# Performance work log

Hardware: AMD Instinct MI355X
Metric: run time of the kernel (lower is better)

## Reference

```python
import jax, jax.numpy as jnp
import numpy as np

N_USERS = 100000
N_ITEMS = 40000
N_NODES = N_USERS + N_ITEMS
D = 64
IMG_DIM = 2048
TXT_DIM = 384
N_EDGES = 1000000
N_LAYERS = 2
ALPHA = 0.2


def setup_inputs() -> dict:
    key = jax.random.key(0)
    ks = jax.random.split(key, 10)
    edge_index = jax.random.randint(ks[0], (2, N_EDGES), 0, N_NODES, dtype=jnp.int64 if jax.config.jax_enable_x64 else jnp.int32)
    edge_weight = jax.random.uniform(ks[1], (N_EDGES, 1), dtype=jnp.float32)
    image_feats = jax.random.normal(ks[2], (N_ITEMS, IMG_DIM), dtype=jnp.float32)
    text_feats = jax.random.normal(ks[3], (N_ITEMS, TXT_DIM), dtype=jnp.float32)
    s_img = 1.0 / np.sqrt(IMG_DIM)
    s_txt = 1.0 / np.sqrt(TXT_DIM)
    image_trs_w = jax.random.uniform(ks[4], (IMG_DIM, D), jnp.float32, -s_img, s_img)
    image_trs_b = jnp.zeros((D,), jnp.float32)
    text_trs_w = jax.random.uniform(ks[5], (TXT_DIM, D), jnp.float32, -s_txt, s_txt)
    text_trs_b = jnp.zeros((D,), jnp.float32)
    image_pref = jax.random.normal(ks[6], (N_USERS, D), jnp.float32) * 0.1
    text_pref = jax.random.normal(ks[7], (N_USERS, D), jnp.float32) * 0.1
    return {
        "edge_index": edge_index,
        "edge_weight": edge_weight,
        "image_feats": image_feats,
        "text_feats": text_feats,
        "image_trs_w": image_trs_w,
        "image_trs_b": image_trs_b,
        "text_trs_w": text_trs_w,
        "text_trs_b": text_trs_b,
        "image_pref": image_pref,
        "text_pref": text_pref,
    }


def _l2_normalize(x):
    # matches F.normalize(x, p=2, dim=1, eps=1e-12)
    n = jnp.linalg.norm(x, axis=1, keepdims=True)
    return x / jnp.maximum(n, 1e-12)


def _propagate(x, src, dst, w):
    # PyG 'add' aggregation: message = x[src] * w, scatter-add into dst
    msgs = x[src] * w  # [E, D]
    return jax.ops.segment_sum(msgs, dst, num_segments=N_NODES)


def reference(edge_index, edge_weight, image_feats, text_feats,
              image_trs_w, image_trs_b, text_trs_w, text_trs_b,
              image_pref, text_pref):
    src, dst = edge_index[0], edge_index[1]

    image_emb = _l2_normalize(image_feats @ image_trs_w + image_trs_b)
    text_emb = _l2_normalize(text_feats @ text_trs_w + text_trs_b)

    ego_img = jnp.concatenate([image_pref, image_emb], axis=0)  # [N, D]
    ego_txt = jnp.concatenate([text_pref, text_emb], axis=0)    # [N, D]

    for _ in range(N_LAYERS):
        ego_img = _propagate(ego_img, src, dst, edge_weight) + ALPHA * ego_img
        ego_txt = _propagate(ego_txt, src, dst, edge_weight) + ALPHA * ego_txt

    # stack final modality embeddings; rows 0:N_USERS are user preferences,
    # N_USERS: are item embeddings (torch.split boundary)
    return jnp.stack([ego_img, ego_txt], axis=0)  # [2, N, D]
```

## Files before the change

kernel.cpp:

```cpp
#include <hip/hip_runtime.h>

#define N_USERS 100000
#define N_ITEMS 40000
#define NN      140000
#define N_EDGES 1000000
#define ALPHA   0.2f

typedef short bf16x8 __attribute__((ext_vector_type(8)));
typedef float f32x4  __attribute__((ext_vector_type(4)));

__device__ __forceinline__ unsigned short f2b(float x) {
    unsigned u = __builtin_bit_cast(unsigned, x);
    unsigned r = (u + 0x7FFFu + ((u >> 16) & 1u)) >> 16;
    return (unsigned short)r;
}
__device__ __forceinline__ unsigned cvtpk(float lo, float hi) {
    unsigned r;
    asm("v_cvt_pk_bf16_f32 %0, %1, %2" : "=v"(r) : "v"(lo), "v"(hi));
    return r;
}
__device__ __forceinline__ float blo(unsigned u) { return __builtin_bit_cast(float, u << 16); }
__device__ __forceinline__ float bhi(unsigned u) { return __builtin_bit_cast(float, u & 0xFFFF0000u); }

__device__ __forceinline__ void gl_lds16(const void* g, void* l) {
    __builtin_amdgcn_global_load_lds(
        (const __attribute__((address_space(1))) void*)g,
        (__attribute__((address_space(3))) void*)l, 16, 0, 0);
}

#define PREP_CP   6250
#define PREP_CI   (PREP_CP + 512)
#define PREP_CT   (PREP_CI + 96)
#define PREP_ALL  (PREP_CT + 3907)

__device__ __forceinline__ int wt_pos(int k, int n) {
    return ((k >> 5) * 4 + (n >> 4)) * 512 + ((((k >> 3) & 3) * 16) + (n & 15)) * 8 + (k & 7);
}

__global__ __launch_bounds__(256)
void prep(const float* __restrict__ imgp, const float* __restrict__ txtp,
          unsigned short* __restrict__ X,
          const float* __restrict__ Wi, short* __restrict__ WtImg,
          const float* __restrict__ Wx, short* __restrict__ WtTxt,
          const int* __restrict__ ei, int* __restrict__ deg,
          int* __restrict__ rank)
{
    int b = blockIdx.x, t = threadIdx.x;
    if (b < PREP_CP) {
        int tid = b * 256 + t;
        if (tid >= N_USERS * 16) return;
        int i  = tid >> 4;
        int c8 = tid & 15;
        const float* src = (c8 < 8) ? &imgp[(size_t)i * 64 + c8 * 8]
                                    : &txtp[(size_t)i * 64 + (c8 - 8) * 8];
        float4 a = *reinterpret_cast<const float4*>(src);
        float4 c = *reinterpret_cast<const float4*>(src + 4);
        int4 o = make_int4((int)cvtpk(a.x, a.y), (int)cvtpk(a.z, a.w),
                           (int)cvtpk(c.x, c.y), (int)cvtpk(c.z, c.w));
        *reinterpret_cast<int4*>(&X[(size_t)i * 128 + c8 * 8]) = o;
    } else if (b < PREP_CI) {
        int tid = (b - PREP_CP) * 256 + t;
        int k = tid >> 6, n = tid & 63;
        WtImg[wt_pos(k, n)] = (short)f2b(Wi[tid]);
    } else if (b < PREP_CT) {
        int tid = (b - PREP_CI) * 256 + t;
        if (tid >= 384 * 64) return;
        int k = tid >> 6, n = tid & 63;
        WtTxt[wt_pos(k, n)] = (short)f2b(Wx[tid]);
    } else {
        int e = (b - PREP_CT) * 256 + t;
        if (e < N_EDGES) {
            int d = ei[N_EDGES + e];
            int r = atomicAdd(&deg[d], 1);
            rank[e] = r;
        }
    }
}

template<int K, int COLOFF>
__device__ __forceinline__
void gemm_body(int bx, const float* __restrict__ A, const short* __restrict__ Wt,
               const float* __restrict__ bias, unsigned short* __restrict__ X,
               float* ldsA, short* ldsB)
{
    constexpr int NT = K / 64;
    const int t    = threadIdx.x;
    const int wid  = t >> 6;
    const int lane = t & 63;
    const int lo   = lane & 15;
    const int g    = lane >> 4;
    const int r0   = bx * 64;

    f32x4 acc[4];
    #pragma unroll
    for (int ct = 0; ct < 4; ++ct) acc[ct] = (f32x4){0.f, 0.f, 0.f, 0.f};

    auto stage = [&](int buf, int kt) {
        int k0 = kt * 64;
        #pragma unroll
        for (int i = 0; i < 4; ++i) {
            int c     = i * 4 + wid;
            int row_t = c * 4 + g;
            int u_log = lo ^ (row_t & 15);
            const float* gp = A + (size_t)(r0 + row_t) * K + k0 + u_log * 4;
            gl_lds16(gp, ldsA + buf * 4096 + c * 256);
        }
        #pragma unroll
        for (int i2 = 0; i2 < 2; ++i2) {
            int c2 = i2 * 4 + wid;
            const short* gp = Wt + ((size_t)kt * 8 + c2) * 512 + lane * 8;
            gl_lds16(gp, ldsB + buf * 4096 + c2 * 512);
        }
    };

    auto compute = [&](int buf) {
        int row_t = wid * 16 + lo;
        const float* baseA = ldsA + buf * 4096 + row_t * 64;
        const short* baseB = ldsB + buf * 4096;
        #pragma unroll
        for (int m = 0; m < 2; ++m) {
            int u0 = (m * 8 + 2 * g) ^ lo;
            int u1 = (m * 8 + 2 * g + 1) ^ lo;
            float4 xa = *reinterpret_cast<const float4*>(baseA + u0 * 4);
            float4 ya = *reinterpret_cast<const float4*>(baseA + u1 * 4);
            int4 ai = make_int4((int)cvtpk(xa.x, xa.y), (int)cvtpk(xa.z, xa.w),
                                (int)cvtpk(ya.x, ya.y), (int)cvtpk(ya.z, ya.w));
            bf16x8 a = __builtin_bit_cast(bf16x8, ai);
            #pragma unroll
            for (int ct = 0; ct < 4; ++ct) {
                int4 w = *reinterpret_cast<const int4*>(baseB + (m * 4 + ct) * 512 + lane * 8);
                bf16x8 bb = __builtin_bit_cast(bf16x8, w);
                acc[ct] = __builtin_amdgcn_mfma_f32_16x16x32_bf16(a, bb, acc[ct], 0, 0, 0);
            }
        }
    };

    stage(0, 0);
    for (int kt = 0; kt < NT; ++kt) {
        if (kt + 1 < NT) {
            stage((kt + 1) & 1, kt + 1);
            asm volatile("s_waitcnt vmcnt(6)" ::: "memory");
        } else {
            asm volatile("s_waitcnt vmcnt(0)" ::: "memory");
        }
        __builtin_amdgcn_s_barrier();
        __builtin_amdgcn_sched_barrier(0);
        compute(kt & 1);
        __builtin_amdgcn_s_barrier();
    }

    float bia[4];
    #pragma unroll
    for (int ct = 0; ct < 4; ++ct) bia[ct] = bias[ct * 16 + lo];

    int r0w = r0 + wid * 16;
    #pragma unroll
    for (int r = 0; r < 4; ++r) {
        float v[4];
        float ss = 0.f;
        #pragma unroll
        for (int ct = 0; ct < 4; ++ct) { v[ct] = acc[ct][r] + bia[ct]; ss += v[ct] * v[ct]; }
        ss += __shfl_xor(ss, 1);
        ss += __shfl_xor(ss, 2);
        ss += __shfl_xor(ss, 4);
        ss += __shfl_xor(ss, 8);
        float sc = 1.0f / fmaxf(sqrtf(ss), 1e-12f);
        int grow = r0w + g * 4 + r;
        unsigned short* dst = &X[(size_t)(N_USERS + grow) * 128 + COLOFF + lo];
        #pragma unroll
        for (int ct = 0; ct < 4; ++ct) dst[ct * 16] = f2b(v[ct] * sc);
    }
}

__global__ __launch_bounds__(256)
void gemm_fill(const float* __restrict__ Ai, const short* __restrict__ WtImg,
               const float* __restrict__ bi,
               const float* __restrict__ Ax, const short* __restrict__ WtTxt,
               const float* __restrict__ bx, unsigned short* __restrict__ X,
               const int* __restrict__ ei, const float* __restrict__ ew,
               const int* __restrict__ row_ptr, const int* __restrict__ rank,
               int2* __restrict__ epk)
{
    __shared__ float ldsA[8192];
    __shared__ __align__(16) short ldsB[8192];
    int b = blockIdx.x;
    if (b < 625)       gemm_body<2048, 0 >(b, Ai, WtImg, bi, X, ldsA, ldsB);
    else if (b < 1250) gemm_body< 384, 64>(b - 625, Ax, WtTxt, bx, X, ldsA, ldsB);
    else {
        int e = (b - 1250) * 256 + threadIdx.x;
        if (e >= N_EDGES) return;
        int s = ei[e];
        int d = ei[N_EDGES + e];
        int p = row_ptr[d] + rank[e];
        epk[p] = make_int2(s, __builtin_bit_cast(int, ew[e]));
    }
}

__global__ void scan1(const int* __restrict__ deg, int* __restrict__ row_ptr,
                      int* __restrict__ blockSums)
{
    __shared__ int ts[256];
    int t = threadIdx.x, b = blockIdx.x;
    int base = b * 1024 + t * 4;
    int v[4]; int s = 0;
    #pragma unroll
    for (int j = 0; j < 4; j++) {
        v[j] = (base + j < NN) ? deg[base + j] : 0;
        s += v[j];
    }
    ts[t] = s;
    __syncthreads();
    for (int off = 1; off < 256; off <<= 1) {
        int x = (t >= off) ? ts[t - off] : 0;
        __syncthreads();
        ts[t] += x;
        __syncthreads();
    }
    int excl = ts[t] - s;
    int run = excl;
    #pragma unroll
    for (int j = 0; j < 4; j++) {
        if (base + j < NN) row_ptr[base + j] = run;
        run += v[j];
    }
    if (t == 255) blockSums[b] = ts[255];
}

__global__ void scan23(const int* __restrict__ blockSums, int* __restrict__ row_ptr)
{
    __shared__ int ts[256];
    int t = threadIdx.x, b = blockIdx.x;
    ts[t] = (t < b) ? blockSums[t] : 0;
    __syncthreads();
    for (int off = 128; off > 0; off >>= 1) {
        if (t < off) ts[t] += ts[t + off];
        __syncthreads();
    }
    int off0 = ts[0];
    int base = b * 1024 + t * 4;
    #pragma unroll
    for (int j = 0; j < 4; j++) {
        int idx = base + j;
        if (idx < NN) row_ptr[idx] += off0;
    }
    if (b == 0 && t == 0) row_ptr[NN] = N_EDGES;
}

template<bool FINAL>
__global__ __launch_bounds__(256)
void propagate(const unsigned short* __restrict__ Xin, const int* __restrict__ row_ptr,
               const int2* __restrict__ epk, void* __restrict__ outv)
{
    int wid  = threadIdx.x >> 6;
    int lane = threadIdx.x & 63;
    int node = blockIdx.x * 4 + wid;
    if (node >= NN) return;
    int e0 = row_ptr[node];
    int e1 = row_ptr[node + 1];
    float accx = 0.f, accy = 0.f;
    for (int base = e0; base < e1; base += 64) {
        int cnt = e1 - base; if (cnt > 64) cnt = 64;
        int sv = 0, wvb = 0;
        if (base + lane < e1) {
            int2 ev = epk[base + lane];
            sv = ev.x; wvb = ev.y;
        }
        float wv = __builtin_bit_cast(float, wvb);
        int i = 0;
        for (; i + 3 < cnt; i += 4) {
            int   s0 = __shfl(sv, i),     s1 = __shfl(sv, i + 1);
            int   s2 = __shfl(sv, i + 2), s3 = __shfl(sv, i + 3);
            float w0 = __shfl(wv, i),     w1 = __shfl(wv, i + 1);
            float w2 = __shfl(wv, i + 2), w3 = __shfl(wv, i + 3);
            unsigned u0 = *reinterpret_cast<const unsigned*>(&Xin[(size_t)s0 * 128 + lane * 2]);
            unsigned u1 = *reinterpret_cast<const unsigned*>(&Xin[(size_t)s1 * 128 + lane * 2]);
            unsigned u2 = *reinterpret_cast<const unsigned*>(&Xin[(size_t)s2 * 128 + lane * 2]);
            unsigned u3 = *reinterpret_cast<const unsigned*>(&Xin[(size_t)s3 * 128 + lane * 2]);
            accx = fmaf(w0, blo(u0), accx); accy = fmaf(w0, bhi(u0), accy);
            accx = fmaf(w1, blo(u1), accx); accy = fmaf(w1, bhi(u1), accy);
            accx = fmaf(w2, blo(u2), accx); accy = fmaf(w2, bhi(u2), accy);
            accx = fmaf(w3, blo(u3), accx); accy = fmaf(w3, bhi(u3), accy);
        }
        for (; i < cnt; ++i) {
            int   s0 = __shfl(sv, i);
            float w0 = __shfl(wv, i);
            unsigned u0 = *reinterpret_cast<const unsigned*>(&Xin[(size_t)s0 * 128 + lane * 2]);
            accx = fmaf(w0, blo(u0), accx); accy = fmaf(w0, bhi(u0), accy);
        }
    }
    unsigned us = *reinterpret_cast<const unsigned*>(&Xin[(size_t)node * 128 + lane * 2]);
    accx += ALPHA * blo(us);
    accy += ALPHA * bhi(us);
    if (!FINAL) {
        unsigned short* out = (unsigned short*)outv;
        *reinterpret_cast<unsigned*>(&out[(size_t)node * 128 + lane * 2]) = cvtpk(accx, accy);
    } else {
        float* out = (float*)outv;
        int d = lane * 2;
        float* dst = (d < 64) ? &out[(size_t)node * 64 + d]
                              : &out[(size_t)NN * 64 + (size_t)node * 64 + (d - 64)];
        *reinterpret_cast<float2*>(dst) = make_float2(accx, accy);
    }
}

extern "C" void kernel_launch(void* const* d_in, const int* in_sizes, int n_in,
                              void* d_out, int out_size, void* d_ws, size_t ws_size,
                              hipStream_t stream)
{
    const int*   ei       = (const int*)d_in[0];
    const float* ew       = (const float*)d_in[1];
    const float* img_feat = (const float*)d_in[2];
    const float* txt_feat = (const float*)d_in[3];
    const float* img_w    = (const float*)d_in[4];
    const float* img_b    = (const float*)d_in[5];
    const float* txt_w    = (const float*)d_in[6];
    const float* txt_b    = (const float*)d_in[7];
    const float* img_pref = (const float*)d_in[8];
    const float* txt_pref = (const float*)d_in[9];
    float* out = (float*)d_out;

    const size_t XBYTES = (size_t)NN * 128 * 2;
    char* ws = (char*)d_ws;
    size_t off = 0;
    auto alloc = [&](size_t bytes) -> void* {
        void* p = ws + off;
        off = (off + bytes + 255) & ~(size_t)255;
        return p;
    };
    unsigned short* Xa = (unsigned short*)alloc(XBYTES);
    unsigned short* Xb = (unsigned short*)alloc(XBYTES);
    int*   deg     = (int*)alloc((size_t)NN * 4);
    int*   row_ptr = (int*)alloc((size_t)(NN + 1) * 4);
    int*   rank    = (int*)alloc((size_t)N_EDGES * 4);
    int2*  epk     = (int2*)alloc((size_t)N_EDGES * 8);
    int*   bsums   = (int*)alloc(256 * 4);
    short* WtImg   = (short*)alloc((size_t)2048 * 64 * 2);
    short* WtTxt   = (short*)alloc((size_t)384 * 64 * 2);

    hipMemsetAsync(deg, 0, (size_t)NN * 4, stream);

    prep<<<PREP_ALL, 256, 0, stream>>>(img_pref, txt_pref, Xa,
                                       img_w, WtImg, txt_w, WtTxt, ei, deg, rank);

    scan1<<<137, 256, 0, stream>>>(deg, row_ptr, bsums);
    scan23<<<137, 256, 0, stream>>>(bsums, row_ptr);

    gemm_fill<<<1250 + 3907, 256, 0, stream>>>(img_feat, WtImg, img_b,
                                               txt_feat, WtTxt, txt_b, Xa,
                                               ei, ew, row_ptr, rank, epk);

    propagate<false><<<35000, 256, 0, stream>>>(Xa, row_ptr, epk, Xb);
    propagate<true ><<<35000, 256, 0, stream>>>(Xb, row_ptr, epk, out);
}
```

Before: 305.4 us.

## Assign 16 lanes per node with 16-byte gathers in propagation

```diff
diff --git a/kernel.cpp b/kernel.cpp
--- a/kernel.cpp
+++ b/kernel.cpp
@@ -251,55 +251,70 @@
 void propagate(const unsigned short* __restrict__ Xin, const int* __restrict__ row_ptr,
                const int2* __restrict__ epk, void* __restrict__ outv)
 {
-    int wid  = threadIdx.x >> 6;
     int lane = threadIdx.x & 63;
-    int node = blockIdx.x * 4 + wid;
-    if (node >= NN) return;
+    int gl   = lane & 15;
+    int gb   = lane & 48;
+    int node = blockIdx.x * 16 + (threadIdx.x >> 4);
     int e0 = row_ptr[node];
     int e1 = row_ptr[node + 1];
-    float accx = 0.f, accy = 0.f;
-    for (int base = e0; base < e1; base += 64) {
-        int cnt = e1 - base; if (cnt > 64) cnt = 64;
+    float a0 = 0.f, a1 = 0.f, a2 = 0.f, a3 = 0.f;
+    float a4 = 0.f, a5 = 0.f, a6 = 0.f, a7 = 0.f;
+
+    for (int base = e0; base < e1; base += 16) {
+        int cnt = e1 - base; if (cnt > 16) cnt = 16;
         int sv = 0, wvb = 0;
-        if (base + lane < e1) {
-            int2 ev = epk[base + lane];
+        if (base + gl < e1) {
+            int2 ev = epk[base + gl];
             sv = ev.x; wvb = ev.y;
         }
         float wv = __builtin_bit_cast(float, wvb);
         int i = 0;
-        for (; i + 3 < cnt; i += 4) {
-            int   s0 = __shfl(sv, i),     s1 = __shfl(sv, i + 1);
-            int   s2 = __shfl(sv, i + 2), s3 = __shfl(sv, i + 3);
-            float w0 = __shfl(wv, i),     w1 = __shfl(wv, i + 1);
-            float w2 = __shfl(wv, i + 2), w3 = __shfl(wv, i + 3);
-            unsigned u0 = *reinterpret_cast<const unsigned*>(&Xin[(size_t)s0 * 128 + lane * 2]);
-            unsigned u1 = *reinterpret_cast<const unsigned*>(&Xin[(size_t)s1 * 128 + lane * 2]);
-            unsigned u2 = *reinterpret_cast<const unsigned*>(&Xin[(size_t)s2 * 128 + lane * 2]);
-            unsigned u3 = *reinterpret_cast<const unsigned*>(&Xin[(size_t)s3 * 128 + lane * 2]);
-            accx = fmaf(w0, blo(u0), accx); accy = fmaf(w0, bhi(u0), accy);
-            accx = fmaf(w1, blo(u1), accx); accy = fmaf(w1, bhi(u1), accy);
-            accx = fmaf(w2, blo(u2), accx); accy = fmaf(w2, bhi(u2), accy);
-            accx = fmaf(w3, blo(u3), accx); accy = fmaf(w3, bhi(u3), accy);
-        }
-        for (; i < cnt; ++i) {
-            int   s0 = __shfl(sv, i);
-            float w0 = __shfl(wv, i);
-            unsigned u0 = *reinterpret_cast<const unsigned*>(&Xin[(size_t)s0 * 128 + lane * 2]);
-            accx = fmaf(w0, blo(u0), accx); accy = fmaf(w0, bhi(u0), accy);
-        }
-    }
-    unsigned us = *reinterpret_cast<const unsigned*>(&Xin[(size_t)node * 128 + lane * 2]);
-    accx += ALPHA * blo(us);
-    accy += ALPHA * bhi(us);
+        for (; i + 1 < cnt; i += 2) {
+            int   s0 = __shfl(sv, gb + i);
+            int   s1 = __shfl(sv, gb + i + 1);
+            float w0 = __shfl(wv, gb + i);
+            float w1 = __shfl(wv, gb + i + 1);
+            uint4 u0 = *reinterpret_cast<const uint4*>(&Xin[(size_t)s0 * 128 + gl * 8]);
+            uint4 u1 = *reinterpret_cast<const uint4*>(&Xin[(size_t)s1 * 128 + gl * 8]);
+            a0 = fmaf(w0, blo(u0.x), a0); a1 = fmaf(w0, bhi(u0.x), a1);
+            a2 = fmaf(w0, blo(u0.y), a2); a3 = fmaf(w0, bhi(u0.y), a3);
+            a4 = fmaf(w0, blo(u0.z), a4); a5 = fmaf(w0, bhi(u0.z), a5);
+            a6 = fmaf(w0, blo(u0.w), a6); a7 = fmaf(w0, bhi(u0.w), a7);
+            a0 = fmaf(w1, blo(u1.x), a0); a1 = fmaf(w1, bhi(u1.x), a1);
+            a2 = fmaf(w1, blo(u1.y), a2); a3 = fmaf(w1, bhi(u1.y), a3);
+            a4 = fmaf(w1, blo(u1.z), a4); a5 = fmaf(w1, bhi(u1.z), a5);
+            a6 = fmaf(w1, blo(u1.w), a6); a7 = fmaf(w1, bhi(u1.w), a7);
+        }
+        if (i < cnt) {
+            int   s0 = __shfl(sv, gb + i);
+            float w0 = __shfl(wv, gb + i);
+            uint4 u0 = *reinterpret_cast<const uint4*>(&Xin[(size_t)s0 * 128 + gl * 8]);
+            a0 = fmaf(w0, blo(u0.x), a0); a1 = fmaf(w0, bhi(u0.x), a1);
+            a2 = fmaf(w0, blo(u0.y), a2); a3 = fmaf(w0, bhi(u0.y), a3);
+            a4 = fmaf(w0, blo(u0.z), a4); a5 = fmaf(w0, bhi(u0.z), a5);
+            a6 = fmaf(w0, blo(u0.w), a6); a7 = fmaf(w0, bhi(u0.w), a7);
+        }
+    }
+
+    uint4 us = *reinterpret_cast<const uint4*>(&Xin[(size_t)node * 128 + gl * 8]);
+    a0 += ALPHA * blo(us.x); a1 += ALPHA * bhi(us.x);
+    a2 += ALPHA * blo(us.y); a3 += ALPHA * bhi(us.y);
+    a4 += ALPHA * blo(us.z); a5 += ALPHA * bhi(us.z);
+    a6 += ALPHA * blo(us.w); a7 += ALPHA * bhi(us.w);
+
     if (!FINAL) {
         unsigned short* out = (unsigned short*)outv;
-        *reinterpret_cast<unsigned*>(&out[(size_t)node * 128 + lane * 2]) = cvtpk(accx, accy);
+        uint4 p;
+        p.x = cvtpk(a0, a1); p.y = cvtpk(a2, a3);
+        p.z = cvtpk(a4, a5); p.w = cvtpk(a6, a7);
+        *reinterpret_cast<uint4*>(&out[(size_t)node * 128 + gl * 8]) = p;
     } else {
         float* out = (float*)outv;
-        int d = lane * 2;
+        int d = gl * 8;
         float* dst = (d < 64) ? &out[(size_t)node * 64 + d]
                               : &out[(size_t)NN * 64 + (size_t)node * 64 + (d - 64)];
-        *reinterpret_cast<float2*>(dst) = make_float2(accx, accy);
+        *reinterpret_cast<float4*>(dst)     = make_float4(a0, a1, a2, a3);
+        *reinterpret_cast<float4*>(dst + 4) = make_float4(a4, a5, a6, a7);
     }
 }
 
@@ -349,6 +364,6 @@
                                                txt_feat, WtTxt, txt_b, Xa,
                                                ei, ew, row_ptr, rank, epk);
 
-    propagate<false><<<35000, 256, 0, stream>>>(Xa, row_ptr, epk, Xb);
-    propagate<true ><<<35000, 256, 0, stream>>>(Xb, row_ptr, epk, out);
-}
+    propagate<false><<<8750, 256, 0, stream>>>(Xa, row_ptr, epk, Xb);
+    propagate<true ><<<8750, 256, 0, stream>>>(Xb, row_ptr, epk, out);
+}
```

Result: faster. 294.4 us (-3.6%).
